# Optimization experiments

Hardware: AMD Instinct MI355X
Metric: run time of the kernel (lower is better)

Reference implementation:

```python
import jax, jax.numpy as jnp
import numpy as np
import math

B, T, D, H, V = 32, 512, 256, 4, 5000
NL = 6          # transformer layers
DUR_CAP = 8     # cap per-token duration so output length is static under jit
T_OUT = 2048    # fixed regulated length (avg duration ~1-2 with small init)


def _layernorm(x, g, b, eps=1e-5):
    m = jnp.mean(x, axis=-1, keepdims=True)
    v = jnp.var(x, axis=-1, keepdims=True)
    return (x - m) * jax.lax.rsqrt(v + eps) * g + b


def _conv1d(x, w, b):
    # x [B,C,T], w [O,I,K] -> [B,O,T], 'same' padding as in torch
    pad = (w.shape[-1] - 1) // 2
    y = jax.lax.conv_general_dilated(x, w, (1,), [(pad, pad)],
                                     dimension_numbers=('NCH', 'OIH', 'NCH'))
    return y + b[None, :, None]


def _pos_encoding(t, d):
    pos = jnp.arange(t, dtype=jnp.float32)[:, None]
    div = jnp.exp(jnp.arange(0, d, 2, dtype=jnp.float32) * (-math.log(10000.0) / d))
    ang = pos * div  # [t, d/2]
    return jnp.stack([jnp.sin(ang), jnp.cos(ang)], axis=-1).reshape(t, d)


def setup_inputs():
    key = jax.random.key(0)
    ks = iter(jax.random.split(key, 64))
    def nrm(shape, s=0.02):
        return jax.random.normal(next(ks), shape, dtype=jnp.float32) * s
    return {
        'text': jax.random.randint(next(ks), (B, T), 0, V, dtype=jnp.int32),
        'emotion': jax.random.normal(next(ks), (B, 1), dtype=jnp.float32),
        'emb': nrm((V, D), 1.0),
        'Wqkv': nrm((NL, D, 3 * D)), 'bqkv': jnp.zeros((NL, 3 * D)),
        'Wo': nrm((NL, D, D)), 'bo': jnp.zeros((NL, D)),
        'W1': nrm((NL, D, 4 * D)), 'b1': jnp.zeros((NL, 4 * D)),
        'W2': nrm((NL, 4 * D, D)), 'b2': jnp.zeros((NL, D)),
        'ln1g': jnp.ones((NL, D)), 'ln1b': jnp.zeros((NL, D)),
        'ln2g': jnp.ones((NL, D)), 'ln2b': jnp.zeros((NL, D)),
        'We1': nrm((1, 64), 0.1), 'be1': jnp.zeros((64,)),
        'We2': nrm((64, D), 0.1), 'be2': jnp.zeros((D,)),
        'dp_w1': nrm((D, D, 3)), 'dp_b1': jnp.zeros((D,)),
        'dp_g1': jnp.ones((D,)), 'dp_bt1': jnp.zeros((D,)),
        'dp_m1': jnp.zeros((D,)), 'dp_v1': jnp.ones((D,)),
        'dp_w2': nrm((D, D, 3)), 'dp_b2': jnp.zeros((D,)),
        'dp_g2': jnp.ones((D,)), 'dp_bt2': jnp.zeros((D,)),
        'dp_m2': jnp.zeros((D,)), 'dp_v2': jnp.ones((D,)),
        'dp_wo': nrm((1, D, 1)), 'dp_bo': jnp.zeros((1,)),
        'dec_w1': nrm((256, D, 5)), 'dec_b1': jnp.zeros((256,)),
        'dec_w2': nrm((128, 256, 5)), 'dec_b2': jnp.zeros((128,)),
        'dec_w3': nrm((1, 128, 5)), 'dec_b3': jnp.zeros((1,)),
    }


def reference(text, emotion, emb, Wqkv, bqkv, Wo, bo, W1, b1, W2, b2,
              ln1g, ln1b, ln2g, ln2b, We1, be1, We2, be2,
              dp_w1, dp_b1, dp_g1, dp_bt1, dp_m1, dp_v1,
              dp_w2, dp_b2, dp_g2, dp_bt2, dp_m2, dp_v2, dp_wo, dp_bo,
              dec_w1, dec_b1, dec_w2, dec_b2, dec_w3, dec_b3):
    dh = D // H
    scale = 1.0 / math.sqrt(dh)
    x = emb[text] + _pos_encoding(T, D)[None]  # [B,T,D]
    # post-norm TransformerEncoder (torch default), relu FFN, eval mode
    for i in range(NL):
        qkv = x @ Wqkv[i] + bqkv[i]
        q, k, v = jnp.split(qkv, 3, axis=-1)
        q = q.reshape(B, T, H, dh); k = k.reshape(B, T, H, dh); v = v.reshape(B, T, H, dh)
        att = jax.nn.softmax(jnp.einsum('bthd,bshd->bhts', q, k) * scale, axis=-1)
        o = jnp.einsum('bhts,bshd->bthd', att, v).reshape(B, T, D) @ Wo[i] + bo[i]
        x = _layernorm(x + o, ln1g[i], ln1b[i])
        ff = jax.nn.relu(x @ W1[i] + b1[i]) @ W2[i] + b2[i]
        x = _layernorm(x + ff, ln2g[i], ln2b[i])
    # EmotionFusion (assumed additive MLP projection, output_dim = 256)
    e = jax.nn.relu(emotion @ We1 + be1) @ We2 + be2  # [B,256]
    fused = x + e[:, None, :]                          # [B,T,D]
    # DurationPredictor (eval: BN with running stats, dropout off)
    def bn(y, g, bt, m, vv):
        return g[None, :, None] * (y - m[None, :, None]) * jax.lax.rsqrt(vv + 1e-5)[None, :, None] + bt[None, :, None]
    h = fused.transpose(0, 2, 1)  # [B,D,T]
    h = bn(jax.nn.relu(_conv1d(h, dp_w1, dp_b1)), dp_g1, dp_bt1, dp_m1, dp_v1)
    h = bn(jax.nn.relu(_conv1d(h, dp_w2, dp_b2)), dp_g2, dp_bt2, dp_m2, dp_v2)
    log_dur = _conv1d(h, dp_wo, dp_bo)[:, 0, :]  # [B,T]
    dur = jnp.clip(jnp.round(jnp.exp(log_dur)), 1, DUR_CAP).astype(jnp.int32)
    dur = jax.lax.stop_gradient(dur)
    # LengthRegulator: repeat token i dur[i] times, zero-pad to T_OUT
    def regulate(xb, db):
        total = jnp.sum(db)
        pad = jnp.maximum(T_OUT - total, 0)
        xe = jnp.concatenate([xb, jnp.zeros((1, D), xb.dtype)], axis=0)
        de = jnp.concatenate([db, pad[None]], axis=0)
        return jnp.repeat(xe, de, axis=0, total_repeat_length=T_OUT)
    reg = jax.vmap(regulate)(fused, dur)  # [B,T_OUT,D]
    # decoder conv stack
    y = reg.transpose(0, 2, 1)
    y = jax.nn.relu(_conv1d(y, dec_w1, dec_b1))
    y = jax.nn.relu(_conv1d(y, dec_w2, dec_b2))
    wav = _conv1d(y, dec_w3, dec_b3)[:, 0, :]  # [B,T_OUT]
    return wav
```

## Files before the change

### kernel.cpp

```cpp
#include <hip/hip_runtime.h>
#include <math.h>

#define NB 32
#define NT 512
#define ND 256
#define NH 4
#define NLAYER 6
#define TOUT 2048

typedef __attribute__((ext_vector_type(8))) short bf16x8;
typedef __attribute__((ext_vector_type(4))) float f32x4;
typedef __attribute__((ext_vector_type(16))) float f32x16;

static __device__ __forceinline__ unsigned short f2b(float f) {
    union { float f; unsigned int u; } x; x.f = f;
    unsigned int u = x.u;
    return (unsigned short)((u + 0x7FFFu + ((u >> 16) & 1u)) >> 16);
}
static __device__ __forceinline__ float b2f(unsigned short s) {
    union { unsigned int u; float f; } x; x.u = ((unsigned int)s) << 16;
    return x.f;
}

#define SW(r) (((r) >> 1) & 3)

#define OFF_X    0ull
#define OFF_FFH  4194304ull
#define OFF_WBT  12582912ull
#define OFF_CWT  14942208ull
#define OFF_QKV  20971520ull
#define OFF_ATTN 33554432ull
#define OFF_PROJ 37748736ull
#define OFF_INT  41951232ull

__global__ __launch_bounds__(256) void embed_kernel(const int* __restrict__ text,
                                                    const float* __restrict__ emb,
                                                    float* __restrict__ x)
{
    const int row = blockIdx.x;
    const int d = threadIdx.x;
    const int t = row & (NT - 1);
    const int id = text[row];
    const int j2 = (d >> 1) * 2;
    const float c = -9.210340371976184f / 256.0f;
    float freq = expf((float)j2 * c);
    float ang = (float)t * freq;
    float pe = (d & 1) ? cosf(ang) : sinf(ang);
    x[(size_t)row * ND + d] = emb[(size_t)id * ND + d] + pe;
}

__global__ __launch_bounds__(256) void wqall_kernel(const float* __restrict__ Wqkv,
                                                    const float* __restrict__ Wo,
                                                    const float* __restrict__ W1,
                                                    const float* __restrict__ W2,
                                                    unsigned short* __restrict__ Wbt)
{
    __shared__ float tile[32][33];
    const int tt = blockIdx.x, layer = blockIdx.y;
    const float* src; int K, N, n0, k0, inLS; size_t outSeg;
    if (tt < 192)      { src = Wqkv; K = 256;  N = 768;  n0 = (tt % 24) * 32; k0 = (tt / 24) * 32; inLS = 196608; outSeg = 0; }
    else if (tt < 256) { int t2 = tt - 192; src = Wo; K = 256; N = 256;  n0 = (t2 & 7) * 32;  k0 = (t2 >> 3) * 32; inLS = 65536;  outSeg = 196608; }
    else if (tt < 512) { int t3 = tt - 256; src = W1; K = 256; N = 1024; n0 = (t3 & 31) * 32; k0 = (t3 >> 5) * 32; inLS = 262144; outSeg = 262144; }
    else               { int t4 = tt - 512; src = W2; K = 1024; N = 256; n0 = (t4 & 7) * 32;  k0 = (t4 >> 3) * 32; inLS = 262144; outSeg = 524288; }
    const float* Wl = src + (size_t)layer * inLS;
    unsigned short* ol = Wbt + (size_t)layer * 786432 + outSeg;
    const int tx = threadIdx.x & 31, ty = threadIdx.x >> 5;
#pragma unroll
    for (int j = 0; j < 4; ++j)
        tile[ty + j * 8][tx] = Wl[(size_t)(k0 + ty + j * 8) * N + n0 + tx];
    __syncthreads();
#pragma unroll
    for (int j = 0; j < 4; ++j)
        ol[(size_t)(n0 + ty + j * 8) * K + k0 + tx] = f2b(tile[tx][ty + j * 8]);
}

__global__ __launch_bounds__(256) void wtransball_kernel(const float* __restrict__ dp_w1,
                                                         const float* __restrict__ dp_w2,
                                                         const float* __restrict__ dec_w1,
                                                         const float* __restrict__ dec_w2,
                                                         unsigned short* __restrict__ cw)
{
    int gid = blockIdx.x * 256 + threadIdx.x;
    if (gid >= 884736) return;
    const float* src; int CIN = 256, COUT, KS, idx;
    if (gid < 196608)      { src = dp_w1;  COUT = 256; KS = 3; idx = gid; }
    else if (gid < 393216) { src = dp_w2;  COUT = 256; KS = 3; idx = gid - 196608; }
    else if (gid < 720896) { src = dec_w1; COUT = 256; KS = 5; idx = gid - 393216; }
    else                   { src = dec_w2; COUT = 128; KS = 5; idx = gid - 720896; }
    int c = idx % CIN;
    int r = idx / CIN;
    int o = r % COUT;
    int k = r / COUT;
    cw[gid] = f2b(src[(o * CIN + c) * KS + k]);
}

template<int NTILE, bool RELU, bool ABF16, bool CBF16, bool VOUT>
__global__ __launch_bounds__(256) void gemmbf_kernel(const void* __restrict__ A_,
                                                     const unsigned short* __restrict__ Bt,
                                                     const float* __restrict__ bias,
                                                     void* __restrict__ C_,
                                                     unsigned short* __restrict__ vt,
                                                     int M, int N, int K)
{
    constexpr int MT = (NTILE == 128) ? 2 : 1;
    __shared__ __align__(16) unsigned short Asb[128 * 32];
    __shared__ __align__(16) unsigned short Bsb[NTILE * 32];
    const int tid = threadIdx.x;
    const int lane = tid & 63, wave = tid >> 6;
    const int ln = lane & 31, hi = lane >> 5;
    const int row0 = blockIdx.y * 128, col0 = blockIdx.x * NTILE;
    const int mOff = (NTILE == 128) ? (wave >> 1) * 64 : wave * 32;
    const int nOff = (NTILE == 128) ? (wave & 1) * 64 : 0;
    const float* Af = (const float*)A_;
    const unsigned short* Ab = (const unsigned short*)A_;
    float* Cf = (float*)C_;
    unsigned short* Cb = (unsigned short*)C_;
    f32x16 acc[MT][2] = {};

    for (int k0 = 0; k0 < K; k0 += 32) {
#pragma unroll
        for (int it = 0; it < 2; ++it) {
            int u = it * 256 + tid;
            int m = u >> 2, blk = u & 3;
            unsigned short s8[8];
            if (ABF16) {
                *(uint4*)s8 = *(const uint4*)&Ab[(size_t)(row0 + m) * K + k0 + blk * 8];
            } else {
                float4 v0 = *(const float4*)&Af[(size_t)(row0 + m) * K + k0 + blk * 8];
                float4 v1 = *(const float4*)&Af[(size_t)(row0 + m) * K + k0 + blk * 8 + 4];
                s8[0] = f2b(v0.x); s8[1] = f2b(v0.y); s8[2] = f2b(v0.z); s8[3] = f2b(v0.w);
                s8[4] = f2b(v1.x); s8[5] = f2b(v1.y); s8[6] = f2b(v1.z); s8[7] = f2b(v1.w);
            }
            *(uint4*)&Asb[m * 32 + ((blk ^ SW(m)) << 3)] = *(uint4*)s8;
        }
#pragma unroll
        for (int it = 0; it < NTILE / 64; ++it) {
            int u = it * 256 + tid;
            int n = u >> 2, blk = u & 3;
            *(uint4*)&Bsb[n * 32 + ((blk ^ SW(n)) << 3)] =
                *(const uint4*)&Bt[(size_t)(col0 + n) * K + k0 + blk * 8];
        }
        __syncthreads();
#pragma unroll
        for (int kh = 0; kh < 2; ++kh) {
            const int kb = kh * 2 + hi;
            bf16x8 af[MT], bfr[2];
#pragma unroll
            for (int mt = 0; mt < MT; ++mt) {
                int r = mOff + mt * 32 + ln;
                af[mt] = *(const bf16x8*)&Asb[r * 32 + ((kb ^ SW(r)) << 3)];
            }
#pragma unroll
            for (int nt = 0; nt < 2; ++nt) {
                int r = nOff + nt * 32 + ln;
                bfr[nt] = *(const bf16x8*)&Bsb[r * 32 + ((kb ^ SW(r)) << 3)];
            }
#pragma unroll
            for (int mt = 0; mt < MT; ++mt)
#pragma unroll
                for (int nt = 0; nt < 2; ++nt)
                    acc[mt][nt] = __builtin_amdgcn_mfma_f32_32x32x16_bf16(
                        af[mt], bfr[nt], acc[mt][nt], 0, 0, 0);
        }
        __syncthreads();
    }
#pragma unroll
    for (int mt = 0; mt < MT; ++mt)
#pragma unroll
        for (int nt = 0; nt < 2; ++nt) {
            int col = col0 + nOff + nt * 32 + ln;
            float bi = bias[col];
#pragma unroll
            for (int g = 0; g < 4; ++g) {
                unsigned short s4[4];
#pragma unroll
                for (int r4 = 0; r4 < 4; ++r4) {
                    int row = row0 + mOff + mt * 32 + hi * 4 + g * 8 + r4;
                    float v = acc[mt][nt][g * 4 + r4] + bi;
                    if (RELU) v = fmaxf(v, 0.f);
                    if (CBF16) { s4[r4] = f2b(v); Cb[(size_t)row * N + col] = s4[r4]; }
                    else       Cf[(size_t)row * N + col] = v;
                }
                if (VOUT && col >= 512) {
                    int rowg = row0 + mOff + mt * 32 + hi * 4 + g * 8;
                    int b = rowg >> 9, t = rowg & (NT - 1);
                    int hh = (col - 512) >> 6, dd = (col - 512) & 63;
                    *(uint2*)&vt[((size_t)(b * NH + hh) * 64 + dd) * NT + t] = *(uint2*)s4;
                }
            }
        }
}

__global__ __launch_bounds__(256) void gemmln_kernel(const unsigned short* __restrict__ A,
                                                     const unsigned short* __restrict__ Bt,
                                                     const float* __restrict__ bias,
                                                     const float* __restrict__ lng,
                                                     const float* __restrict__ lnb,
                                                     float* __restrict__ x,
                                                     int K)
{
    __shared__ __align__(16) unsigned short Asb[64 * 32];
    __shared__ __align__(16) unsigned short Bsb[256 * 32];
    __shared__ float sred[64][2][2];
    const int tid = threadIdx.x;
    const int lane = tid & 63, wave = tid >> 6;
    const int ln = lane & 31, hi = lane >> 5;
    const int row0 = blockIdx.x * 64;
    const int mOff = (wave >> 1) * 32;
    const int colbase = (wave & 1) * 128;
    f32x16 acc[4] = {};

    for (int k0 = 0; k0 < K; k0 += 32) {
        {
            int m = tid >> 2, blk = tid & 3;
            *(uint4*)&Asb[m * 32 + ((blk ^ SW(m)) << 3)] =
                *(const uint4*)&A[(size_t)(row0 + m) * K + k0 + blk * 8];
        }
#pragma unroll
        for (int it = 0; it < 4; ++it) {
            int u = it * 256 + tid;
            int n = u >> 2, blk = u & 3;
            *(uint4*)&Bsb[n * 32 + ((blk ^ SW(n)) << 3)] =
                *(const uint4*)&Bt[(size_t)n * K + k0 + blk * 8];
        }
        __syncthreads();
#pragma unroll
        for (int kh = 0; kh < 2; ++kh) {
            const int kb = kh * 2 + hi;
            int r = mOff + ln;
            bf16x8 af = *(const bf16x8*)&Asb[r * 32 + ((kb ^ SW(r)) << 3)];
#pragma unroll
            for (int nt = 0; nt < 4; ++nt) {
                int rb = colbase + nt * 32 + ln;
                bf16x8 bfr = *(const bf16x8*)&Bsb[rb * 32 + ((kb ^ SW(rb)) << 3)];
                acc[nt] = __builtin_amdgcn_mfma_f32_32x32x16_bf16(af, bfr, acc[nt], 0, 0, 0);
            }
        }
        __syncthreads();
    }

    float bi[4], gv[4], bv[4];
#pragma unroll
    for (int nt = 0; nt < 4; ++nt) {
        int col = colbase + nt * 32 + ln;
        bi[nt] = bias[col]; gv[nt] = lng[col]; bv[nt] = lnb[col];
    }
#pragma unroll
    for (int g = 0; g < 4; ++g)
#pragma unroll
        for (int r4 = 0; r4 < 4; ++r4) {
            int rl = mOff + hi * 4 + g * 8 + r4;
            size_t base = (size_t)(row0 + rl) * ND + colbase + ln;
#pragma unroll
            for (int nt = 0; nt < 4; ++nt)
                acc[nt][g * 4 + r4] += bi[nt] + x[base + nt * 32];
        }
#pragma unroll
    for (int g = 0; g < 4; ++g)
#pragma unroll
        for (int r4 = 0; r4 < 4; ++r4) {
            int i = g * 4 + r4;
            float ps = acc[0][i] + acc[1][i] + acc[2][i] + acc[3][i];
            float ps2 = acc[0][i] * acc[0][i] + acc[1][i] * acc[1][i]
                      + acc[2][i] * acc[2][i] + acc[3][i] * acc[3][i];
#pragma unroll
            for (int o = 1; o < 32; o <<= 1) {
                ps += __shfl_xor(ps, o);
                ps2 += __shfl_xor(ps2, o);
            }
            if (ln == 0) {
                int rl = mOff + hi * 4 + g * 8 + r4;
                sred[rl][wave & 1][0] = ps;
                sred[rl][wave & 1][1] = ps2;
            }
        }
    __syncthreads();
#pragma unroll
    for (int g = 0; g < 4; ++g)
#pragma unroll
        for (int r4 = 0; r4 < 4; ++r4) {
            int i = g * 4 + r4;
            int rl = mOff + hi * 4 + g * 8 + r4;
            float s = sred[rl][0][0] + sred[rl][1][0];
            float s2 = sred[rl][0][1] + sred[rl][1][1];
            float m = s * (1.0f / 256.0f);
            float var = fmaxf(s2 * (1.0f / 256.0f) - m * m, 0.0f);
            float rinv = 1.0f / sqrtf(var + 1e-5f);
            size_t base = (size_t)(row0 + rl) * ND + colbase + ln;
#pragma unroll
            for (int nt = 0; nt < 4; ++nt)
                x[base + nt * 32] = (acc[nt][i] - m) * rinv * gv[nt] + bv[nt];
        }
}

__global__ __launch_bounds__(256, 2) void attn3_kernel(const unsigned short* __restrict__ qkv,
                                                       const unsigned short* __restrict__ vt,
                                                       unsigned short* __restrict__ out)
{
    __shared__ __align__(16) unsigned short sP[4][32 * 64];
    const int tid = threadIdx.x;
    const int lane = tid & 63, wave = tid >> 6;
    const int ln = lane & 31, hi = lane >> 5;
    const int h = blockIdx.y, b = blockIdx.z;
    const int q0 = blockIdx.x * 128 + wave * 32;
    const size_t base = (size_t)b * NT * 768;
    const int qoff = h * 64;
    const unsigned short* vbh = vt + (size_t)(b * NH + h) * 64 * NT;

    bf16x8 qf[4];
#pragma unroll
    for (int s = 0; s < 4; ++s)
        qf[s] = *(const bf16x8*)&qkv[base + (size_t)(q0 + ln) * 768 + qoff + s * 16 + hi * 8];

    float mrow[16], lrow[16];
#pragma unroll
    for (int i = 0; i < 16; ++i) { mrow[i] = -1e30f; lrow[i] = 0.f; }
    f32x16 oacc[2] = {};
    const float sc = 0.18033688011112042f;
    const int i0 = (ln & 3) | (((ln >> 3) & 3) << 2);
    const bool own = (((ln >> 2) & 1) == hi);
    unsigned short* Pw = &sP[wave][0];

    for (int ch = 0; ch < 8; ++ch) {
        const int s0 = ch * 64;
        f32x16 sacc[2] = {};
#pragma unroll
        for (int ct = 0; ct < 2; ++ct)
#pragma unroll
            for (int s = 0; s < 4; ++s) {
                bf16x8 kf = *(const bf16x8*)&qkv[base + (size_t)(s0 + ct * 32 + ln) * 768
                                                 + 256 + qoff + s * 16 + hi * 8];
                sacc[ct] = __builtin_amdgcn_mfma_f32_32x32x16_bf16(qf[s], kf, sacc[ct], 0, 0, 0);
            }
        float alpha[16];
#pragma unroll
        for (int i = 0; i < 16; ++i) {
            float s20 = sacc[0][i] * sc, s21 = sacc[1][i] * sc;
            float mx = fmaxf(s20, s21);
#pragma unroll
            for (int o = 1; o < 32; o <<= 1) mx = fmaxf(mx, __shfl_xor(mx, o));
            float mn = fmaxf(mrow[i], mx);
            alpha[i] = exp2f(mrow[i] - mn);
            mrow[i] = mn;
            float p0 = exp2f(s20 - mn);
            float p1 = exp2f(s21 - mn);
            sacc[0][i] = p0; sacc[1][i] = p1;
            float rs = p0 + p1;
#pragma unroll
            for (int o = 1; o < 32; o <<= 1) rs += __shfl_xor(rs, o);
            lrow[i] = lrow[i] * alpha[i] + rs;
        }
#pragma unroll
        for (int ct = 0; ct < 2; ++ct) {
            int kb = ct * 4 + (ln >> 3), k7 = ln & 7;
#pragma unroll
            for (int i = 0; i < 16; ++i) {
                int q = (i & 3) + 8 * (i >> 2) + 4 * hi;
                Pw[q * 64 + (((kb ^ (q & 7)) << 3) | k7)] = f2b(sacc[ct][i]);
            }
        }
        __syncthreads();
        {
            float av = alpha[i0];
            float ao = __shfl_xor(av, 32);
            float aq = own ? av : ao;
#pragma unroll
            for (int ct = 0; ct < 2; ++ct)
#pragma unroll
                for (int i = 0; i < 16; ++i)
                    oacc[ct][i] *= aq;
        }
#pragma unroll
        for (int s = 0; s < 4; ++s) {
            bf16x8 pf = *(const bf16x8*)&Pw[ln * 64 + (((s * 2 + hi) ^ (ln & 7)) << 3)];
#pragma unroll
            for (int ct = 0; ct < 2; ++ct) {
                bf16x8 vf = *(const bf16x8*)&vbh[(size_t)(ct * 32 + ln) * NT + s0 + s * 16 + hi * 8];
                oacc[ct] = __builtin_amdgcn_mfma_f32_32x32x16_bf16(vf, pf, oacc[ct], 0, 0, 0);
            }
        }
        __syncthreads();
    }
    float lv = lrow[i0];
    float lo = __shfl_xor(lv, 32);
    float linv = 1.0f / (own ? lv : lo);
    const int q = q0 + ln;
#pragma unroll
    for (int ct = 0; ct < 2; ++ct)
#pragma unroll
        for (int i = 0; i < 16; ++i) {
            int d = ct * 32 + (i & 3) + 8 * (i >> 2) + 4 * hi;
            out[(size_t)(b * NT + q) * ND + qoff + d] = f2b(oacc[ct][i] * linv);
        }
}

__global__ __launch_bounds__(256) void fuse_kernel(const float* __restrict__ emo,
                                                   const float* __restrict__ We1,
                                                   const float* __restrict__ be1,
                                                   const float* __restrict__ We2,
                                                   const float* __restrict__ be2,
                                                   float* __restrict__ x)
{
    const int row = blockIdx.x;
    const int d = threadIdx.x;
    const float em = emo[row >> 9];
    float acc = be2[d];
    for (int j = 0; j < 64; ++j) {
        float h = fmaxf(em * We1[j] + be1[j], 0.0f);
        acc = fmaf(h, We2[j * ND + d], acc);
    }
    x[(size_t)row * ND + d] += acc;
}

template<int CIN, int KS, bool IN_BF16, bool OUT_BF16, bool BN>
__global__ __launch_bounds__(256) void convk_kernel(const void* __restrict__ in_,
                                                    const unsigned short* __restrict__ wtb,
                                                    const float* __restrict__ bias,
                                                    const float* __restrict__ bng,
                                                    const float* __restrict__ bnb,
                                                    const float* __restrict__ bnm,
                                                    const float* __restrict__ bnv,
                                                    void* __restrict__ out_,
                                                    int T, int COUT)
{
    constexpr int PAD = (KS - 1) / 2;
    constexpr int TEXT = 256 + KS - 1;
    __shared__ __align__(16) unsigned short Asb[TEXT * 32];
    __shared__ __align__(16) unsigned short Bsb[KS * 64 * 32];
    const int tid = threadIdx.x;
    const int lane = tid & 63, wave = tid >> 6;
    const int ln = lane & 31, hi = lane >> 5;
    const int b = blockIdx.z;
    const int t0 = blockIdx.x * 256;
    const int o0 = blockIdx.y * 64;
    const int mOff = wave * 64;
    const float* inf = (const float*)in_;
    const unsigned short* inb = (const unsigned short*)in_;
    float* outf = (float*)out_;
    unsigned short* outb = (unsigned short*)out_;
    f32x16 acc[2][2] = {};

    for (int cc = 0; cc < CIN; cc += 32) {
        for (int u = tid; u < TEXT * 4; u += 256) {
            int t = u >> 2, blk = u & 3;
            int tg = t0 - PAD + t;
            unsigned short s8[8] = {0, 0, 0, 0, 0, 0, 0, 0};
            if (tg >= 0 && tg < T) {
                if (IN_BF16) {
                    *(uint4*)s8 = *(const uint4*)&inb[((size_t)(b * T) + tg) * CIN + cc + blk * 8];
                } else {
                    float4 v0 = *(const float4*)&inf[((size_t)(b * T) + tg) * CIN + cc + blk * 8];
                    float4 v1 = *(const float4*)&inf[((size_t)(b * T) + tg) * CIN + cc + blk * 8 + 4];
                    s8[0] = f2b(v0.x); s8[1] = f2b(v0.y); s8[2] = f2b(v0.z); s8[3] = f2b(v0.w);
                    s8[4] = f2b(v1.x); s8[5] = f2b(v1.y); s8[6] = f2b(v1.z); s8[7] = f2b(v1.w);
                }
            }
            *(uint4*)&Asb[t * 32 + ((blk ^ SW(t)) << 3)] = *(uint4*)s8;
        }
        for (int u = tid; u < KS * 256; u += 256) {
            int row = u >> 2, blk = u & 3;
            int k = row >> 6, o = row & 63;
            *(uint4*)&Bsb[row * 32 + ((blk ^ SW(row)) << 3)] =
                *(const uint4*)&wtb[((size_t)k * COUT + o0 + o) * CIN + cc + blk * 8];
        }
        __syncthreads();
#pragma unroll
        for (int kh = 0; kh < 2; ++kh) {
            const int kb = kh * 2 + hi;
#pragma unroll
            for (int tap = 0; tap < KS; ++tap) {
                bf16x8 af[2];
#pragma unroll
                for (int mt = 0; mt < 2; ++mt) {
                    int r = mOff + mt * 32 + ln + tap;
                    af[mt] = *(const bf16x8*)&Asb[r * 32 + ((kb ^ SW(r)) << 3)];
                }
#pragma unroll
                for (int nt = 0; nt < 2; ++nt) {
                    int rb = tap * 64 + nt * 32 + ln;
                    bf16x8 bfr = *(const bf16x8*)&Bsb[rb * 32 + ((kb ^ SW(rb)) << 3)];
#pragma unroll
                    for (int mt = 0; mt < 2; ++mt)
                        acc[mt][nt] = __builtin_amdgcn_mfma_f32_32x32x16_bf16(
                            af[mt], bfr, acc[mt][nt], 0, 0, 0);
                }
            }
        }
        __syncthreads();
    }
#pragma unroll
    for (int nt = 0; nt < 2; ++nt) {
        int col = o0 + nt * 32 + ln;
        float bi = bias[col];
        float scv = 1.f, shv = 0.f;
        if (BN) {
            scv = bng[col] / sqrtf(bnv[col] + 1e-5f);
            shv = bnb[col] - bnm[col] * scv;
        }
#pragma unroll
        for (int mt = 0; mt < 2; ++mt)
#pragma unroll
            for (int g = 0; g < 4; ++g)
#pragma unroll
                for (int r4 = 0; r4 < 4; ++r4) {
                    int row = t0 + mOff + mt * 32 + hi * 4 + g * 8 + r4;
                    float v = fmaxf(acc[mt][nt][g * 4 + r4] + bi, 0.f);
                    if (BN) v = v * scv + shv;
                    if (OUT_BF16) outb[((size_t)(b * T) + row) * COUT + col] = f2b(v);
                    else          outf[((size_t)(b * T) + row) * COUT + col] = v;
                }
    }
}

__global__ __launch_bounds__(256) void reg_kernel(const float* __restrict__ x,
                                                  const int* __restrict__ tok,
                                                  unsigned short* __restrict__ reg)
{
    const int wave = threadIdx.x >> 6, lane = threadIdx.x & 63;
    const int row = blockIdx.x * 4 + wave;
    const int tk = tok[row];
    const int b = row >> 11;
    const int c4 = lane * 4;
    unsigned short s4[4] = {0, 0, 0, 0};
    if (tk >= 0) {
        float4 v = *(const float4*)&x[((size_t)(b * NT) + tk) * ND + c4];
        s4[0] = f2b(v.x); s4[1] = f2b(v.y); s4[2] = f2b(v.z); s4[3] = f2b(v.w);
    }
    *(uint2*)&reg[(size_t)row * ND + c4] = *(uint2*)s4;
}

__global__ __launch_bounds__(256) void dur_kernel(const float* __restrict__ h2,
                                                  const float* __restrict__ wo,
                                                  const float* __restrict__ bo,
                                                  int* __restrict__ dur)
{
    const int wave = threadIdx.x >> 6, lane = threadIdx.x & 63;
    const int row = blockIdx.x * 4 + wave;
    const int c4 = lane * 4;
    float4 h = *(const float4*)&h2[(size_t)row * ND + c4];
    float4 w4 = *(const float4*)&wo[c4];
    float s = h.x * w4.x + h.y * w4.y + h.z * w4.z + h.w * w4.w;
#pragma unroll
    for (int o = 1; o < 64; o <<= 1) s += __shfl_xor(s, o);
    if (lane == 0) {
        float d = rintf(expf(s + bo[0]));
        d = fminf(fmaxf(d, 1.0f), 8.0f);
        dur[row] = (int)d;
    }
}

__global__ __launch_bounds__(256) void scantok_kernel(const int* __restrict__ dur,
                                                      int* __restrict__ tok)
{
    __shared__ int st[NT];
    __shared__ int tot;
    const int b = blockIdx.x, tid = threadIdx.x;
    if (tid == 0) {
        int a = 0;
        for (int t = 0; t < NT; ++t) { st[t] = a; a += dur[b * NT + t]; }
        tot = a;
    }
    __syncthreads();
    for (int p = tid; p < TOUT; p += 256) {
        int res = -1;
        if (p < tot) {
            int lo = 0, hi = NT - 1;
            while (lo < hi) {
                int mid = (lo + hi + 1) >> 1;
                if (st[mid] <= p) lo = mid; else hi = mid - 1;
            }
            res = lo;
        }
        tok[b * TOUT + p] = res;
    }
}

__global__ __launch_bounds__(256) void conv3_kernel(const unsigned short* __restrict__ in,
                                                    const float* __restrict__ w,
                                                    const float* __restrict__ bias,
                                                    float* __restrict__ out)
{
    const int wave = threadIdx.x >> 6, lane = threadIdx.x & 63;
    const int gid = blockIdx.x * 4 + wave;
    const int b = gid >> 11, t = gid & (TOUT - 1);
    const int c = lane * 2;
    float w0[5], w1[5];
#pragma unroll
    for (int k = 0; k < 5; ++k) { w0[k] = w[c * 5 + k]; w1[k] = w[(c + 1) * 5 + k]; }
    float acc = 0.f;
#pragma unroll
    for (int k = 0; k < 5; ++k) {
        int t2 = t + k - 2;
        if (t2 < 0 || t2 >= TOUT) continue;
        unsigned int u = *(const unsigned int*)&in[((size_t)(b * TOUT) + t2) * 128 + c];
        acc = fmaf(b2f((unsigned short)(u & 0xFFFF)), w0[k], acc);
        acc = fmaf(b2f((unsigned short)(u >> 16)), w1[k], acc);
    }
#pragma unroll
    for (int o = 1; o < 64; o <<= 1) acc += __shfl_xor(acc, o);
    if (lane == 0) out[gid] = acc + bias[0];
}

extern "C" void kernel_launch(void* const* d_in, const int* in_sizes, int n_in,
                              void* d_out, int out_size, void* d_ws, size_t ws_size,
                              hipStream_t stream)
{
    const int*   text    = (const int*)d_in[0];
    const float* emotion = (const float*)d_in[1];
    const float* emb     = (const float*)d_in[2];
    const float* Wqkv    = (const float*)d_in[3];
    const float* bqkv    = (const float*)d_in[4];
    const float* Wo      = (const float*)d_in[5];
    const float* bo      = (const float*)d_in[6];
    const float* W1      = (const float*)d_in[7];
    const float* b1      = (const float*)d_in[8];
    const float* W2      = (const float*)d_in[9];
    const float* b2      = (const float*)d_in[10];
    const float* ln1g    = (const float*)d_in[11];
    const float* ln1b    = (const float*)d_in[12];
    const float* ln2g    = (const float*)d_in[13];
    const float* ln2b    = (const float*)d_in[14];
    const float* We1     = (const float*)d_in[15];
    const float* be1     = (const float*)d_in[16];
    const float* We2     = (const float*)d_in[17];
    const float* be2     = (const float*)d_in[18];
    const float* dp_w1   = (const float*)d_in[19];
    const float* dp_b1   = (const float*)d_in[20];
    const float* dp_g1   = (const float*)d_in[21];
    const float* dp_bt1  = (const float*)d_in[22];
    const float* dp_m1   = (const float*)d_in[23];
    const float* dp_v1   = (const float*)d_in[24];
    const float* dp_w2   = (const float*)d_in[25];
    const float* dp_b2   = (const float*)d_in[26];
    const float* dp_g2   = (const float*)d_in[27];
    const float* dp_bt2  = (const float*)d_in[28];
    const float* dp_m2   = (const float*)d_in[29];
    const float* dp_v2   = (const float*)d_in[30];
    const float* dp_wo   = (const float*)d_in[31];
    const float* dp_bo   = (const float*)d_in[32];
    const float* dec_w3  = (const float*)d_in[37];
    const float* dec_b1  = (const float*)d_in[34];
    const float* dec_b2  = (const float*)d_in[36];
    const float* dec_b3  = (const float*)d_in[38];

    float* ws   = (float*)d_ws;
    float* x    = ws + OFF_X;
    unsigned short* ffhB = (unsigned short*)(ws + OFF_FFH);
    unsigned short* Wbt  = (unsigned short*)(ws + OFF_WBT);
    unsigned short* cw   = (unsigned short*)(ws + OFF_CWT);
    unsigned short* wtbdp1 = cw;
    unsigned short* wtbdp2 = cw + 196608;
    unsigned short* wtb1   = cw + 393216;
    unsigned short* wtb2   = cw + 720896;
    unsigned short* qkvB = (unsigned short*)(ws + OFF_QKV);
    unsigned short* vtb  = qkvB + 12582912;
    unsigned short* regB = qkvB;
    float* attb = ws + OFF_ATTN;
    float* prjb = ws + OFF_PROJ;
    unsigned short* attbB = (unsigned short*)attb;
    unsigned short* h1b  = (unsigned short*)attb;
    unsigned short* d1b  = ffhB;
    unsigned short* d2b  = (unsigned short*)attb;
    int*   ip     = (int*)(ws + OFF_INT);
    int*   durb   = ip;
    int*   tokb   = ip + 16384;

    const int M = NB * NT;

    embed_kernel<<<M, 256, 0, stream>>>(text, emb, x);
    wqall_kernel<<<dim3(768, 6), 256, 0, stream>>>(Wqkv, Wo, W1, W2, Wbt);
    wtransball_kernel<<<3456, 256, 0, stream>>>(dp_w1, dp_w2,
                                                (const float*)d_in[33], (const float*)d_in[35], cw);

    for (int l = 0; l < NLAYER; ++l) {
        const unsigned short* WQ  = Wbt + (size_t)l * 786432;
        const unsigned short* WO  = WQ + 196608;
        const unsigned short* WF1 = WQ + 262144;
        const unsigned short* WF2 = WQ + 524288;
        gemmbf_kernel<128, false, false, true, true><<<dim3(6, 128), 256, 0, stream>>>(
            x, WQ, bqkv + l * 768, qkvB, vtb, M, 768, 256);
        attn3_kernel<<<dim3(NT / 128, NH, NB), 256, 0, stream>>>(qkvB, vtb, attbB);
        gemmln_kernel<<<M / 64, 256, 0, stream>>>(
            attbB, WO, bo + l * 256, ln1g + l * ND, ln1b + l * ND, x, 256);
        gemmbf_kernel<128, true, false, true, false><<<dim3(8, 128), 256, 0, stream>>>(
            x, WF1, b1 + l * 1024, ffhB, nullptr, M, 1024, 256);
        gemmln_kernel<<<M / 64, 256, 0, stream>>>(
            ffhB, WF2, b2 + l * 256, ln2g + l * ND, ln2b + l * ND, x, 1024);
    }

    fuse_kernel<<<M, 256, 0, stream>>>(emotion, We1, be1, We2, be2, x);

    convk_kernel<256, 3, false, true, true><<<dim3(2, 4, NB), 256, 0, stream>>>(
        x, wtbdp1, dp_b1, dp_g1, dp_bt1, dp_m1, dp_v1, h1b, NT, 256);
    convk_kernel<256, 3, true, false, true><<<dim3(2, 4, NB), 256, 0, stream>>>(
        h1b, wtbdp2, dp_b2, dp_g2, dp_bt2, dp_m2, dp_v2, prjb, NT, 256);
    dur_kernel<<<M / 4, 256, 0, stream>>>(prjb, dp_wo, dp_bo, durb);
    scantok_kernel<<<NB, 256, 0, stream>>>(durb, tokb);

    reg_kernel<<<NB * TOUT / 4, 256, 0, stream>>>(x, tokb, regB);
    convk_kernel<256, 5, true, true, false><<<dim3(TOUT / 256, 4, NB), 256, 0, stream>>>(
        regB, wtb1, dec_b1, nullptr, nullptr, nullptr, nullptr, d1b, TOUT, 256);
    convk_kernel<256, 5, true, true, false><<<dim3(TOUT / 256, 2, NB), 256, 0, stream>>>(
        d1b, wtb2, dec_b2, nullptr, nullptr, nullptr, nullptr, d2b, TOUT, 128);
    conv3_kernel<<<NB * TOUT / 4, 256, 0, stream>>>(d2b, dec_w3, dec_b3, (float*)d_out);
}
```

Before: 1.473 ms.

## Prefetch next K-chunk into registers and widen GEMM K tile to 64

The GEMM, GEMM+LayerNorm and conv kernels now issue global loads for the next K chunk into registers before the MFMA loop on the current chunk, and write them to LDS after the compute. The goal is to hide global memory latency behind the matrix math. The two GEMM kernels also double the K step from 32 to 64, with an 8-way XOR swizzle, which halves the number of barriers per tile. The cost is more registers and LDS, which may lower occupancy, and the kernels now assume K is a multiple of 64.

```diff
diff --git a/kernel.cpp b/kernel.cpp
--- a/kernel.cpp
+++ b/kernel.cpp
@@ -22,7 +22,8 @@
     return x.f;
 }
 
-#define SW(r) (((r) >> 1) & 3)
+#define SW(r)  (((r) >> 1) & 3)
+#define SW8(r) ((r) & 7)
 
 #define OFF_X    0ull
 #define OFF_FFH  4194304ull
@@ -103,8 +104,9 @@
                                                      int M, int N, int K)
 {
     constexpr int MT = (NTILE == 128) ? 2 : 1;
-    __shared__ __align__(16) unsigned short Asb[128 * 32];
-    __shared__ __align__(16) unsigned short Bsb[NTILE * 32];
+    constexpr int BUNITS = NTILE / 32;
+    __shared__ __align__(16) unsigned short Asb[128 * 64];
+    __shared__ __align__(16) unsigned short Bsb[NTILE * 64];
     const int tid = threadIdx.x;
     const int lane = tid & 63, wave = tid >> 6;
     const int ln = lane & 31, hi = lane >> 5;
@@ -116,44 +118,66 @@
     float* Cf = (float*)C_;
     unsigned short* Cb = (unsigned short*)C_;
     f32x16 acc[MT][2] = {};
-
-    for (int k0 = 0; k0 < K; k0 += 32) {
-#pragma unroll
-        for (int it = 0; it < 2; ++it) {
-            int u = it * 256 + tid;
-            int m = u >> 2, blk = u & 3;
-            unsigned short s8[8];
+    uint4 aR[4], bR[BUNITS];
+
+    auto loadA = [&](int k0) {
+#pragma unroll
+        for (int it = 0; it < 4; ++it) {
+            int u = it * 256 + tid;
+            int m = u >> 3, blk = u & 7;
             if (ABF16) {
-                *(uint4*)s8 = *(const uint4*)&Ab[(size_t)(row0 + m) * K + k0 + blk * 8];
+                aR[it] = *(const uint4*)&Ab[(size_t)(row0 + m) * K + k0 + blk * 8];
             } else {
                 float4 v0 = *(const float4*)&Af[(size_t)(row0 + m) * K + k0 + blk * 8];
                 float4 v1 = *(const float4*)&Af[(size_t)(row0 + m) * K + k0 + blk * 8 + 4];
+                unsigned short s8[8];
                 s8[0] = f2b(v0.x); s8[1] = f2b(v0.y); s8[2] = f2b(v0.z); s8[3] = f2b(v0.w);
                 s8[4] = f2b(v1.x); s8[5] = f2b(v1.y); s8[6] = f2b(v1.z); s8[7] = f2b(v1.w);
-            }
-            *(uint4*)&Asb[m * 32 + ((blk ^ SW(m)) << 3)] = *(uint4*)s8;
-        }
-#pragma unroll
-        for (int it = 0; it < NTILE / 64; ++it) {
-            int u = it * 256 + tid;
-            int n = u >> 2, blk = u & 3;
-            *(uint4*)&Bsb[n * 32 + ((blk ^ SW(n)) << 3)] =
-                *(const uint4*)&Bt[(size_t)(col0 + n) * K + k0 + blk * 8];
-        }
+                aR[it] = *(uint4*)s8;
+            }
+        }
+    };
+    auto loadB = [&](int k0) {
+#pragma unroll
+        for (int it = 0; it < BUNITS; ++it) {
+            int u = it * 256 + tid;
+            int n = u >> 3, blk = u & 7;
+            bR[it] = *(const uint4*)&Bt[(size_t)(col0 + n) * K + k0 + blk * 8];
+        }
+    };
+    auto storeAB = [&]() {
+#pragma unroll
+        for (int it = 0; it < 4; ++it) {
+            int u = it * 256 + tid;
+            int m = u >> 3, blk = u & 7;
+            *(uint4*)&Asb[m * 64 + ((blk ^ SW8(m)) << 3)] = aR[it];
+        }
+#pragma unroll
+        for (int it = 0; it < BUNITS; ++it) {
+            int u = it * 256 + tid;
+            int n = u >> 3, blk = u & 7;
+            *(uint4*)&Bsb[n * 64 + ((blk ^ SW8(n)) << 3)] = bR[it];
+        }
+    };
+
+    loadA(0); loadB(0); storeAB();
+    const int nc = K >> 6;
+    for (int c = 0; c < nc; ++c) {
         __syncthreads();
-#pragma unroll
-        for (int kh = 0; kh < 2; ++kh) {
+        if (c + 1 < nc) { loadA((c + 1) << 6); loadB((c + 1) << 6); }
+#pragma unroll
+        for (int kh = 0; kh < 4; ++kh) {
             const int kb = kh * 2 + hi;
             bf16x8 af[MT], bfr[2];
 #pragma unroll
             for (int mt = 0; mt < MT; ++mt) {
                 int r = mOff + mt * 32 + ln;
-                af[mt] = *(const bf16x8*)&Asb[r * 32 + ((kb ^ SW(r)) << 3)];
+                af[mt] = *(const bf16x8*)&Asb[r * 64 + ((kb ^ SW8(r)) << 3)];
             }
 #pragma unroll
             for (int nt = 0; nt < 2; ++nt) {
                 int r = nOff + nt * 32 + ln;
-                bfr[nt] = *(const bf16x8*)&Bsb[r * 32 + ((kb ^ SW(r)) << 3)];
+                bfr[nt] = *(const bf16x8*)&Bsb[r * 64 + ((kb ^ SW8(r)) << 3)];
             }
 #pragma unroll
             for (int mt = 0; mt < MT; ++mt)
@@ -163,6 +187,7 @@
                         af[mt], bfr[nt], acc[mt][nt], 0, 0, 0);
         }
         __syncthreads();
+        if (c + 1 < nc) storeAB();
     }
 #pragma unroll
     for (int mt = 0; mt < MT; ++mt)
@@ -199,8 +224,8 @@
                                                      float* __restrict__ x,
                                                      int K)
 {
-    __shared__ __align__(16) unsigned short Asb[64 * 32];
-    __shared__ __align__(16) unsigned short Bsb[256 * 32];
+    __shared__ __align__(16) unsigned short Asb[64 * 64];
+    __shared__ __align__(16) unsigned short Bsb[256 * 64];
     __shared__ float sred[64][2][2];
     const int tid = threadIdx.x;
     const int lane = tid & 63, wave = tid >> 6;
@@ -209,34 +234,58 @@
     const int mOff = (wave >> 1) * 32;
     const int colbase = (wave & 1) * 128;
     f32x16 acc[4] = {};
-
-    for (int k0 = 0; k0 < K; k0 += 32) {
-        {
-            int m = tid >> 2, blk = tid & 3;
-            *(uint4*)&Asb[m * 32 + ((blk ^ SW(m)) << 3)] =
-                *(const uint4*)&A[(size_t)(row0 + m) * K + k0 + blk * 8];
-        }
-#pragma unroll
-        for (int it = 0; it < 4; ++it) {
-            int u = it * 256 + tid;
-            int n = u >> 2, blk = u & 3;
-            *(uint4*)&Bsb[n * 32 + ((blk ^ SW(n)) << 3)] =
-                *(const uint4*)&Bt[(size_t)n * K + k0 + blk * 8];
-        }
+    uint4 aR[2], bR[8];
+
+    auto loadA = [&](int k0) {
+#pragma unroll
+        for (int it = 0; it < 2; ++it) {
+            int u = it * 256 + tid;
+            int m = u >> 3, blk = u & 7;
+            aR[it] = *(const uint4*)&A[(size_t)(row0 + m) * K + k0 + blk * 8];
+        }
+    };
+    auto loadB = [&](int k0) {
+#pragma unroll
+        for (int it = 0; it < 8; ++it) {
+            int u = it * 256 + tid;
+            int n = u >> 3, blk = u & 7;
+            bR[it] = *(const uint4*)&Bt[(size_t)n * K + k0 + blk * 8];
+        }
+    };
+    auto storeAB = [&]() {
+#pragma unroll
+        for (int it = 0; it < 2; ++it) {
+            int u = it * 256 + tid;
+            int m = u >> 3, blk = u & 7;
+            *(uint4*)&Asb[m * 64 + ((blk ^ SW8(m)) << 3)] = aR[it];
+        }
+#pragma unroll
+        for (int it = 0; it < 8; ++it) {
+            int u = it * 256 + tid;
+            int n = u >> 3, blk = u & 7;
+            *(uint4*)&Bsb[n * 64 + ((blk ^ SW8(n)) << 3)] = bR[it];
+        }
+    };
+
+    loadA(0); loadB(0); storeAB();
+    const int nc = K >> 6;
+    for (int c = 0; c < nc; ++c) {
         __syncthreads();
-#pragma unroll
-        for (int kh = 0; kh < 2; ++kh) {
+        if (c + 1 < nc) { loadA((c + 1) << 6); loadB((c + 1) << 6); }
+#pragma unroll
+        for (int kh = 0; kh < 4; ++kh) {
             const int kb = kh * 2 + hi;
             int r = mOff + ln;
-            bf16x8 af = *(const bf16x8*)&Asb[r * 32 + ((kb ^ SW(r)) << 3)];
+            bf16x8 af = *(const bf16x8*)&Asb[r * 64 + ((kb ^ SW8(r)) << 3)];
 #pragma unroll
             for (int nt = 0; nt < 4; ++nt) {
                 int rb = colbase + nt * 32 + ln;
-                bf16x8 bfr = *(const bf16x8*)&Bsb[rb * 32 + ((kb ^ SW(rb)) << 3)];
+                bf16x8 bfr = *(const bf16x8*)&Bsb[rb * 64 + ((kb ^ SW8(rb)) << 3)];
                 acc[nt] = __builtin_amdgcn_mfma_f32_32x32x16_bf16(af, bfr, acc[nt], 0, 0, 0);
             }
         }
         __syncthreads();
+        if (c + 1 < nc) storeAB();
     }
 
     float bi[4], gv[4], bv[4];
@@ -425,6 +474,7 @@
 {
     constexpr int PAD = (KS - 1) / 2;
     constexpr int TEXT = 256 + KS - 1;
+    constexpr int AUNITS = (TEXT * 4 + 255) / 256;
     __shared__ __align__(16) unsigned short Asb[TEXT * 32];
     __shared__ __align__(16) unsigned short Bsb[KS * 64 * 32];
     const int tid = threadIdx.x;
@@ -439,9 +489,13 @@
     float* outf = (float*)out_;
     unsigned short* outb = (unsigned short*)out_;
     f32x16 acc[2][2] = {};
-
-    for (int cc = 0; cc < CIN; cc += 32) {
-        for (int u = tid; u < TEXT * 4; u += 256) {
+    uint4 aR[AUNITS], bR[KS];
+
+    auto loadA = [&](int cc) {
+#pragma unroll
+        for (int it = 0; it < AUNITS; ++it) {
+            int u = it * 256 + tid;
+            if (u >= TEXT * 4) continue;
             int t = u >> 2, blk = u & 3;
             int tg = t0 - PAD + t;
             unsigned short s8[8] = {0, 0, 0, 0, 0, 0, 0, 0};
@@ -455,15 +509,38 @@
                     s8[4] = f2b(v1.x); s8[5] = f2b(v1.y); s8[6] = f2b(v1.z); s8[7] = f2b(v1.w);
                 }
             }
-            *(uint4*)&Asb[t * 32 + ((blk ^ SW(t)) << 3)] = *(uint4*)s8;
-        }
-        for (int u = tid; u < KS * 256; u += 256) {
+            aR[it] = *(uint4*)s8;
+        }
+    };
+    auto loadB = [&](int cc) {
+#pragma unroll
+        for (int it = 0; it < KS; ++it) {
+            int u = it * 256 + tid;
             int row = u >> 2, blk = u & 3;
             int k = row >> 6, o = row & 63;
-            *(uint4*)&Bsb[row * 32 + ((blk ^ SW(row)) << 3)] =
-                *(const uint4*)&wtb[((size_t)k * COUT + o0 + o) * CIN + cc + blk * 8];
-        }
+            bR[it] = *(const uint4*)&wtb[((size_t)k * COUT + o0 + o) * CIN + cc + blk * 8];
+        }
+    };
+    auto storeAB = [&]() {
+#pragma unroll
+        for (int it = 0; it < AUNITS; ++it) {
+            int u = it * 256 + tid;
+            if (u >= TEXT * 4) continue;
+            int t = u >> 2, blk = u & 3;
+            *(uint4*)&Asb[t * 32 + ((blk ^ SW(t)) << 3)] = aR[it];
+        }
+#pragma unroll
+        for (int it = 0; it < KS; ++it) {
+            int u = it * 256 + tid;
+            int row = u >> 2, blk = u & 3;
+            *(uint4*)&Bsb[row * 32 + ((blk ^ SW(row)) << 3)] = bR[it];
+        }
+    };
+
+    loadA(0); loadB(0); storeAB();
+    for (int cc = 0; cc < CIN; cc += 32) {
         __syncthreads();
+        if (cc + 32 < CIN) { loadA(cc + 32); loadB(cc + 32); }
 #pragma unroll
         for (int kh = 0; kh < 2; ++kh) {
             const int kb = kh * 2 + hi;
@@ -487,6 +564,7 @@
             }
         }
         __syncthreads();
+        if (cc + 32 < CIN) storeAB();
     }
 #pragma unroll
     for (int nt = 0; nt < 2; ++nt) {
```

New measurement: 2.124 ms. 44.2% more time.
